# Optimization experiments

Measured on AMD Instinct MI355X. Metric: run time of the kernel, lower is better.

The kernel has to match this reference:

```python
import jax, jax.numpy as jnp
import numpy as np

N = 50000          # nodes
E = 800000         # edges (no self loops; self loops added in reference)
D = 128            # in_channels == out_channels (required by index_add into x)
HEADS = 1
NEG_SLOPE = 0.2
NUM_LABELS = 7


def setup_inputs() -> dict:
    key = jax.random.key(0)
    k0, k1, k2, k3, k4, k5 = jax.random.split(key, 6)
    x = jax.random.normal(k0, (N, D), dtype=jnp.float32)
    # edges guaranteed self-loop-free (remove_self_loops is then a no-op)
    src = jax.random.randint(k1, (E,), 0, N, dtype=jnp.int32)
    off = jax.random.randint(k2, (E,), 1, N, dtype=jnp.int32)
    dst = (src + off) % N
    edge_index = jnp.stack([src, dst])  # [2, E]
    node_label = jax.random.randint(k3, (N,), 0, 8, dtype=jnp.int32)  # 0 = inactive, 1..7 active
    glorot = float(np.sqrt(6.0 / (D + D)))
    weight_id = jax.random.uniform(k4, (NUM_LABELS, D, D), jnp.float32, -glorot, glorot)
    ga = float(np.sqrt(6.0 / (HEADS * 2 * D + 1)))
    att = jax.random.uniform(k5, (1, HEADS, 2 * D), jnp.float32, -ga, ga)
    return {"x": x, "edge_index": edge_index, "node_label": node_label,
            "weight_id": weight_id, "att": att}


def reference(x, edge_index, node_label, weight_id, att):
    n, d = x.shape
    # --- per-label identity transform: ox = x + W_{label-1} x for labels 1..7 ---
    y = jnp.einsum('nd,kdo->nko', x, weight_id)           # [N, 7, D]
    valid = (node_label >= 1) & (node_label <= NUM_LABELS)
    idx = jnp.clip(node_label - 1, 0, NUM_LABELS - 1)
    delta = jnp.take_along_axis(y, idx[:, None, None], axis=1)[:, 0]  # [N, D]
    ox = x + jnp.where(valid[:, None], delta, jnp.zeros_like(delta))
    # --- add self loops (input has none) ---
    loops = jnp.arange(n, dtype=edge_index.dtype)
    src = jnp.concatenate([edge_index[0], loops])
    dst = jnp.concatenate([edge_index[1], loops])
    # --- GAT message: gather, attention score, edge softmax over dst ---
    x_j = ox[src].reshape(-1, HEADS, d)                   # [Et, 1, D]
    x_i = ox[dst].reshape(-1, HEADS, d)
    alpha = (x_i * att[:, :, :d]).sum(-1) + (x_j * att[:, :, d:]).sum(-1)  # [Et, 1]
    alpha = jax.nn.leaky_relu(alpha, NEG_SLOPE)
    amax = jax.ops.segment_max(alpha, dst, num_segments=n)  # every node has a self loop
    alpha = jnp.exp(alpha - amax[dst])
    denom = jax.ops.segment_sum(alpha, dst, num_segments=n)
    alpha = alpha / (denom[dst] + 1e-16)
    # dropout p=0 (eval) -> no-op
    msg = (x_j * alpha[:, :, None]).reshape(-1, HEADS * d)  # concat=True, heads=1
    out = jax.ops.segment_sum(msg, dst, num_segments=n)     # [N, D]; bias=False
    return out
```

## Files before the change

### kernel.cpp

```cpp
#include <hip/hip_runtime.h>
#include <math.h>

#define N_NODES 50000
#define N_EDGES 800000
#define DIM 128
#define SCAN_BLOCKS ((N_NODES + 255) / 256)
#define DEG_CAP 48
#define BINS ((N_NODES + 255) / 256)
#define BIN_CAP 8192
#define EA_CHUNK 4096

#define PREP_ELEMS (N_NODES * DIM / 4 + 7 * DIM * DIM)
#define PREP_BLOCKS ((PREP_ELEMS + 255) / 256)
#define P1_GRID (BINS + PREP_BLOCKS + SCAN_BLOCKS)

#define TR_BLOCKS 784
#define P2_GRID (BINS + TR_BLOCKS)

typedef __attribute__((ext_vector_type(8))) short short8;
typedef __attribute__((ext_vector_type(4))) float floatx4;

__device__ __forceinline__ unsigned short f2bf(float f) {
    unsigned int u = __float_as_uint(f);
    unsigned int r = (u + 0x7fff + ((u >> 16) & 1)) >> 16;
    return (unsigned short)r;
}
__device__ __forceinline__ float bf2f_lo(unsigned int v) { return __uint_as_float(v << 16); }
__device__ __forceinline__ float bf2f_hi(unsigned int v) { return __uint_as_float(v & 0xffff0000u); }

__global__ __launch_bounds__(256) void phase1_kernel(
        const float* __restrict__ x, const int* __restrict__ src, const int* __restrict__ dst,
        const int* __restrict__ label, const float* __restrict__ W,
        unsigned short* __restrict__ oxh, unsigned short* __restrict__ Wt,
        int* __restrict__ bin_cur, unsigned int* __restrict__ binned,
        int* __restrict__ lab_cnt, int* __restrict__ node_list) {
    int t = threadIdx.x;
    int blk = blockIdx.x;

    if (blk < BINS) {
        __shared__ int hist[BINS], base_s[BINS], rank[BINS];
        for (int i = t; i < BINS; i += 256) { hist[i] = 0; rank[i] = 0; }
        __syncthreads();
        int e0 = blk * EA_CHUNK;
        int e1 = e0 + EA_CHUNK; if (e1 > N_EDGES) e1 = N_EDGES;
        for (int e = e0 + t; e < e1; e += 256) atomicAdd(&hist[dst[e] >> 8], 1);
        __syncthreads();
        for (int i = t; i < BINS; i += 256)
            base_s[i] = (hist[i] > 0) ? atomicAdd(&bin_cur[i], hist[i]) : 0;
        __syncthreads();
        for (int e = e0 + t; e < e1; e += 256) {
            int d = dst[e];
            int b = d >> 8;
            int r = atomicAdd(&rank[b], 1);
            int slot = base_s[b] + r;
            if (slot < BIN_CAP)
                binned[(size_t)b * BIN_CAP + slot] = (unsigned int)(src[e] | ((d & 255) << 16));
        }
    } else if (blk < BINS + PREP_BLOCKS) {
        int i = (blk - BINS) * 256 + t;
        const int nx = N_NODES * DIM / 4;
        if (i < nx) {
            float4 v = ((const float4*)x)[i];
            ushort4 o;
            o.x = f2bf(v.x); o.y = f2bf(v.y); o.z = f2bf(v.z); o.w = f2bf(v.w);
            ((ushort4*)oxh)[i] = o;
        } else {
            int j = i - nx;
            if (j < 7 * DIM * DIM) {
                int b = j >> 14;
                int d = (j >> 7) & 127;
                int c = j & 127;
                Wt[((size_t)b * DIM + c) * DIM + d] = f2bf(W[j]);
            }
        }
    } else {
        __shared__ int lcnt[8], lbase[8], lrank[8];
        int i = (blk - BINS - PREP_BLOCKS) * 256 + t;
        if (t < 8) { lcnt[t] = 0; lrank[t] = 0; }
        __syncthreads();
        int b = -1;
        if (i < N_NODES) {
            int lab = label[i];
            b = (lab >= 1 && lab <= 7) ? (lab - 1) : 7;
            atomicAdd(&lcnt[b], 1);
        }
        __syncthreads();
        if (t < 8) lbase[t] = (lcnt[t] > 0) ? atomicAdd(&lab_cnt[t], lcnt[t]) : 0;
        __syncthreads();
        if (i < N_NODES) {
            int r = atomicAdd(&lrank[b], 1);
            node_list[(size_t)b * N_NODES + lbase[b] + r] = i;
        }
    }
}

__global__ __launch_bounds__(256) void phase2_kernel(
        const float* __restrict__ x, const float* __restrict__ att,
        const int* __restrict__ lab_cnt, const int* __restrict__ node_list,
        const unsigned short* __restrict__ Wt,
        const int* __restrict__ bin_cur, const unsigned int* __restrict__ binned,
        unsigned short* __restrict__ oxh, float* __restrict__ ai, float* __restrict__ aj,
        int* __restrict__ cnt, unsigned short* __restrict__ bucket) {
    int t = threadIdx.x;
    int blk = blockIdx.x;

    if (blk < BINS) {
        __shared__ int hist[256], off[256], cur[256], sc[256];
        __shared__ unsigned short srt[BIN_CAP];
        int b = blk;
        int m = bin_cur[b]; if (m > BIN_CAP) m = BIN_CAP;
        const unsigned int* bp = binned + (size_t)b * BIN_CAP;

        hist[t] = 0; cur[t] = 0;
        __syncthreads();
        for (int i = t; i < m; i += 256) atomicAdd(&hist[(bp[i] >> 16) & 255], 1);
        __syncthreads();
        sc[t] = hist[t];
        __syncthreads();
        #pragma unroll
        for (int d = 1; d < 256; d <<= 1) {
            int add = (t >= d) ? sc[t - d] : 0;
            __syncthreads();
            sc[t] += add;
            __syncthreads();
        }
        off[t] = sc[t] - hist[t];
        __syncthreads();
        for (int i = t; i < m; i += 256) {
            unsigned int v = bp[i];
            int ln = (v >> 16) & 255;
            int r = atomicAdd(&cur[ln], 1);
            srt[off[ln] + r] = (unsigned short)(v & 0xFFFF);
        }
        __syncthreads();
        int n = b * 256 + t;
        if (n < N_NODES) {
            int deg = hist[t];
            if (deg > DEG_CAP) deg = DEG_CAP;
            cnt[n] = deg;
            int o = off[t];
            unsigned short* brow = bucket + (size_t)n * DEG_CAP;
            for (int k = 0; k < deg; k++) brow[k] = srt[o + k];
        }
    } else {
        int wv = t >> 6;
        int lane = t & 63;
        int tile = (blk - BINS) * 4 + wv;

        int b = 0, base = 0, tcnt = 0;
        for (; b < 8; b++) {
            int c = lab_cnt[b];
            int nt = (c + 15) >> 4;
            if (tile < nt) { base = b * N_NODES + tile * 16; tcnt = c - tile * 16; break; }
            tile -= nt;
        }
        if (b == 8) return;
        if (tcnt > 16) tcnt = 16;

        int m = lane & 15;
        int quad = lane >> 4;

        floatx4 acc[8];
        #pragma unroll
        for (int nt = 0; nt < 8; nt++) acc[nt] = (floatx4){0.f, 0.f, 0.f, 0.f};

        if (b < 7) {
            int mm = (m < tcnt) ? m : 0;
            int nodeA = node_list[base + mm];
            const unsigned short* xrow = oxh + (size_t)nodeA * DIM;
            short8 afrag[4];
            #pragma unroll
            for (int kk = 0; kk < 4; kk++)
                afrag[kk] = *(const short8*)(xrow + kk * 32 + quad * 8);

            const unsigned short* WtB = Wt + (size_t)b * DIM * DIM;
            #pragma unroll
            for (int kk = 0; kk < 4; kk++) {
                #pragma unroll
                for (int nt = 0; nt < 8; nt++) {
                    short8 bfrag = *(const short8*)(WtB + (size_t)(nt * 16 + m) * DIM + kk * 32 + quad * 8);
                    acc[nt] = __builtin_amdgcn_mfma_f32_16x16x32_bf16(afrag[kk], bfrag, acc[nt], 0, 0, 0);
                }
            }
        }

        int nodes[4];
        #pragma unroll
        for (int r = 0; r < 4; r++) {
            int rw = quad * 4 + r;
            nodes[r] = node_list[base + ((rw < tcnt) ? rw : 0)];
        }
        float pi[4] = {0.f, 0.f, 0.f, 0.f};
        float pj[4] = {0.f, 0.f, 0.f, 0.f};
        #pragma unroll
        for (int nt = 0; nt < 8; nt++) {
            int c = nt * 16 + m;
            float a1 = att[c];
            float a2 = att[DIM + c];
            #pragma unroll
            for (int r = 0; r < 4; r++) {
                int rw = quad * 4 + r;
                if (rw < tcnt) {
                    float xv = x[(size_t)nodes[r] * DIM + c];
                    float v = (b < 7) ? (acc[nt][r] + xv) : xv;
                    if (b < 7) oxh[(size_t)nodes[r] * DIM + c] = f2bf(v);
                    pi[r] += v * a1;
                    pj[r] += v * a2;
                }
            }
        }
        #pragma unroll
        for (int r = 0; r < 4; r++) {
            #pragma unroll
            for (int off = 1; off < 16; off <<= 1) {
                pi[r] += __shfl_xor(pi[r], off, 64);
                pj[r] += __shfl_xor(pj[r], off, 64);
            }
            int rw = quad * 4 + r;
            if (m == 0 && rw < tcnt) {
                ai[nodes[r]] = pi[r];
                aj[nodes[r]] = pj[r];
            }
        }
    }
}

__global__ __launch_bounds__(256) void gather6_kernel(
        const int* __restrict__ cnt, const unsigned short* __restrict__ bucket,
        const float* __restrict__ ai, const float* __restrict__ aj,
        const uint4* __restrict__ tab,
        float* __restrict__ out) {
    int wv = threadIdx.x >> 6;
    int lane = threadIdx.x & 63;
    int n = blockIdx.x * 4 + wv;
    if (n >= N_NODES) return;
    int deg = cnt[n];
    if (deg > DEG_CAP) deg = DEG_CAP;
    const unsigned short* row = bucket + (size_t)n * DEG_CAP;
    float ain = ai[n];

    float a = -INFINITY;
    int s = n;
    if (lane < deg) {
        s = row[lane];
        a = ain + aj[s];
        a = (a > 0.0f) ? a : 0.2f * a;
    } else if (lane == deg) {
        a = ain + aj[n];
        a = (a > 0.0f) ? a : 0.2f * a;
    }
    float mx = a;
    #pragma unroll
    for (int off = 32; off > 0; off >>= 1) mx = fmaxf(mx, __shfl_xor(mx, off, 64));
    float w = expf(a - mx);
    float ssum = w;
    #pragma unroll
    for (int off = 32; off > 0; off >>= 1) ssum += __shfl_xor(ssum, off, 64);
    float wn = w / (ssum + 1e-16f);
    float wsf = __shfl(wn, deg, 64);

    int g = lane >> 4;
    int cl = lane & 15;
    float ac0 = 0.f, ac1 = 0.f, ac2 = 0.f, ac3 = 0.f;
    float ac4 = 0.f, ac5 = 0.f, ac6 = 0.f, ac7 = 0.f;

    if (g == 0) {
        uint4 v = tab[(size_t)n * 16 + cl];
        ac0 += wsf * bf2f_lo(v.x); ac1 += wsf * bf2f_hi(v.x);
        ac2 += wsf * bf2f_lo(v.y); ac3 += wsf * bf2f_hi(v.y);
        ac4 += wsf * bf2f_lo(v.z); ac5 += wsf * bf2f_hi(v.z);
        ac6 += wsf * bf2f_lo(v.w); ac7 += wsf * bf2f_hi(v.w);
    }

    int niter = (deg + 3) >> 2;
    for (int k = 0; k < niter; k++) {
        int i = g + 4 * k;
        bool valid = (i < deg);
        int idx = valid ? i : 0;
        float wi = __shfl(wn, idx, 64);
        int   si = __shfl(s, idx, 64);
        if (!valid) wi = 0.0f;
        uint4 v = tab[(size_t)si * 16 + cl];
        ac0 += wi * bf2f_lo(v.x); ac1 += wi * bf2f_hi(v.x);
        ac2 += wi * bf2f_lo(v.y); ac3 += wi * bf2f_hi(v.y);
        ac4 += wi * bf2f_lo(v.z); ac5 += wi * bf2f_hi(v.z);
        ac6 += wi * bf2f_lo(v.w); ac7 += wi * bf2f_hi(v.w);
    }

    #pragma unroll
    for (int off = 16; off < 64; off <<= 1) {
        ac0 += __shfl_xor(ac0, off, 64); ac1 += __shfl_xor(ac1, off, 64);
        ac2 += __shfl_xor(ac2, off, 64); ac3 += __shfl_xor(ac3, off, 64);
        ac4 += __shfl_xor(ac4, off, 64); ac5 += __shfl_xor(ac5, off, 64);
        ac6 += __shfl_xor(ac6, off, 64); ac7 += __shfl_xor(ac7, off, 64);
    }
    if (g == 0) {
        float* op = out + (size_t)n * DIM + cl * 8;
        float4 o0; o0.x = ac0; o0.y = ac1; o0.z = ac2; o0.w = ac3;
        float4 o1; o1.x = ac4; o1.y = ac5; o1.z = ac6; o1.w = ac7;
        *(float4*)op = o0;
        *(float4*)(op + 4) = o1;
    }
}

extern "C" void kernel_launch(void* const* d_in, const int* in_sizes, int n_in,
                              void* d_out, int out_size, void* d_ws, size_t ws_size,
                              hipStream_t stream) {
    const float* x     = (const float*)d_in[0];
    const int*   ei    = (const int*)d_in[1];
    const int*   label = (const int*)d_in[2];
    const float* W     = (const float*)d_in[3];
    const float* att   = (const float*)d_in[4];
    float* out = (float*)d_out;

    const int* src = ei;
    const int* dst = ei + N_EDGES;

    char* w = (char*)d_ws;
    unsigned short* oxh    = (unsigned short*)w; w += sizeof(unsigned short) * (size_t)N_NODES * DIM;
    unsigned short* Wt     = (unsigned short*)w; w += sizeof(unsigned short) * 7 * DIM * DIM;
    unsigned short* bucket = (unsigned short*)w; w += sizeof(unsigned short) * (size_t)N_NODES * DEG_CAP;
    unsigned int*   binned = (unsigned int*)w;   w += sizeof(unsigned int) * (size_t)BINS * BIN_CAP;
    float* ai        = (float*)w;  w += sizeof(float) * N_NODES;
    float* aj        = (float*)w;  w += sizeof(float) * N_NODES;
    int*   cnt       = (int*)w;    w += sizeof(int) * N_NODES;
    int*   node_list = (int*)w;    w += sizeof(int) * (size_t)8 * N_NODES;
    int*   lab_cnt   = (int*)w;    w += sizeof(int) * 8;
    int*   bin_cur   = (int*)w;    w += sizeof(int) * BINS;

    hipMemsetAsync(lab_cnt, 0, sizeof(int) * (8 + BINS), stream);

    phase1_kernel<<<P1_GRID, 256, 0, stream>>>(x, src, dst, label, W,
                                               oxh, Wt, bin_cur, binned, lab_cnt, node_list);

    phase2_kernel<<<P2_GRID, 256, 0, stream>>>(x, att, lab_cnt, node_list, Wt,
                                               bin_cur, binned, oxh, ai, aj, cnt, bucket);

    gather6_kernel<<<(N_NODES + 3) / 4, 256, 0, stream>>>(cnt, bucket, ai, aj,
                                                          (const uint4*)oxh, out);
}
```

Baseline: 166.5 us.

## Replace two-pass binned CSR build with direct global-atomic bucket scatter

The edge bucketing drops the two-stage bin/local-sort path and has each edge do a global atomicAdd on a per-destination counter, writing its source straight into that node's fixed-capacity bucket. The separate x-to-bf16 conversion pass is also removed: the transform kernel converts x rows to bf16 on the fly for the MFMA A fragments and writes oxh for every node. This removes a kernel's worth of staging traffic and the intermediate binned buffer, at the cost of 800k contended global atomics and unordered bucket contents. The gather kernel now reads the raw counter, which can exceed DEG_CAP, and relies on its own clamp.

New measurement: 191.9 us. 15.3% more time.

```diff
diff --git a/kernel.cpp b/kernel.cpp
--- a/kernel.cpp
+++ b/kernel.cpp
@@ -4,18 +4,14 @@
 #define N_NODES 50000
 #define N_EDGES 800000
 #define DIM 128
-#define SCAN_BLOCKS ((N_NODES + 255) / 256)
 #define DEG_CAP 48
-#define BINS ((N_NODES + 255) / 256)
-#define BIN_CAP 8192
-#define EA_CHUNK 4096
-
-#define PREP_ELEMS (N_NODES * DIM / 4 + 7 * DIM * DIM)
-#define PREP_BLOCKS ((PREP_ELEMS + 255) / 256)
-#define P1_GRID (BINS + PREP_BLOCKS + SCAN_BLOCKS)
+
+#define SC_BLOCKS ((N_EDGES + 255) / 256)
+#define LB_BLOCKS ((N_NODES + 255) / 256)
+#define WT_BLOCKS ((7 * DIM * DIM + 255) / 256)
+#define K1_GRID (SC_BLOCKS + LB_BLOCKS + WT_BLOCKS)
 
 #define TR_BLOCKS 784
-#define P2_GRID (BINS + TR_BLOCKS)
 
 typedef __attribute__((ext_vector_type(8))) short short8;
 typedef __attribute__((ext_vector_type(4))) float floatx4;
@@ -28,54 +24,26 @@
 __device__ __forceinline__ float bf2f_lo(unsigned int v) { return __uint_as_float(v << 16); }
 __device__ __forceinline__ float bf2f_hi(unsigned int v) { return __uint_as_float(v & 0xffff0000u); }
 
-__global__ __launch_bounds__(256) void phase1_kernel(
-        const float* __restrict__ x, const int* __restrict__ src, const int* __restrict__ dst,
+__global__ __launch_bounds__(256) void build_kernel(
+        const int* __restrict__ src, const int* __restrict__ dst,
         const int* __restrict__ label, const float* __restrict__ W,
-        unsigned short* __restrict__ oxh, unsigned short* __restrict__ Wt,
-        int* __restrict__ bin_cur, unsigned int* __restrict__ binned,
+        unsigned short* __restrict__ Wt,
+        int* __restrict__ cur, unsigned short* __restrict__ bucket,
         int* __restrict__ lab_cnt, int* __restrict__ node_list) {
     int t = threadIdx.x;
     int blk = blockIdx.x;
 
-    if (blk < BINS) {
-        __shared__ int hist[BINS], base_s[BINS], rank[BINS];
-        for (int i = t; i < BINS; i += 256) { hist[i] = 0; rank[i] = 0; }
-        __syncthreads();
-        int e0 = blk * EA_CHUNK;
-        int e1 = e0 + EA_CHUNK; if (e1 > N_EDGES) e1 = N_EDGES;
-        for (int e = e0 + t; e < e1; e += 256) atomicAdd(&hist[dst[e] >> 8], 1);
-        __syncthreads();
-        for (int i = t; i < BINS; i += 256)
-            base_s[i] = (hist[i] > 0) ? atomicAdd(&bin_cur[i], hist[i]) : 0;
-        __syncthreads();
-        for (int e = e0 + t; e < e1; e += 256) {
+    if (blk < SC_BLOCKS) {
+        int e = blk * 256 + t;
+        if (e < N_EDGES) {
             int d = dst[e];
-            int b = d >> 8;
-            int r = atomicAdd(&rank[b], 1);
-            int slot = base_s[b] + r;
-            if (slot < BIN_CAP)
-                binned[(size_t)b * BIN_CAP + slot] = (unsigned int)(src[e] | ((d & 255) << 16));
-        }
-    } else if (blk < BINS + PREP_BLOCKS) {
-        int i = (blk - BINS) * 256 + t;
-        const int nx = N_NODES * DIM / 4;
-        if (i < nx) {
-            float4 v = ((const float4*)x)[i];
-            ushort4 o;
-            o.x = f2bf(v.x); o.y = f2bf(v.y); o.z = f2bf(v.z); o.w = f2bf(v.w);
-            ((ushort4*)oxh)[i] = o;
-        } else {
-            int j = i - nx;
-            if (j < 7 * DIM * DIM) {
-                int b = j >> 14;
-                int d = (j >> 7) & 127;
-                int c = j & 127;
-                Wt[((size_t)b * DIM + c) * DIM + d] = f2bf(W[j]);
-            }
-        }
-    } else {
+            int pos = atomicAdd(&cur[d], 1);
+            if (pos < DEG_CAP)
+                bucket[(size_t)d * DEG_CAP + pos] = (unsigned short)src[e];
+        }
+    } else if (blk < SC_BLOCKS + LB_BLOCKS) {
         __shared__ int lcnt[8], lbase[8], lrank[8];
-        int i = (blk - BINS - PREP_BLOCKS) * 256 + t;
+        int i = (blk - SC_BLOCKS) * 256 + t;
         if (t < 8) { lcnt[t] = 0; lrank[t] = 0; }
         __syncthreads();
         int b = -1;
@@ -91,136 +59,108 @@
             int r = atomicAdd(&lrank[b], 1);
             node_list[(size_t)b * N_NODES + lbase[b] + r] = i;
         }
-    }
-}
-
-__global__ __launch_bounds__(256) void phase2_kernel(
+    } else {
+        int j = (blk - SC_BLOCKS - LB_BLOCKS) * 256 + t;
+        if (j < 7 * DIM * DIM) {
+            int b = j >> 14;
+            int d = (j >> 7) & 127;
+            int c = j & 127;
+            Wt[((size_t)b * DIM + c) * DIM + d] = f2bf(W[j]);
+        }
+    }
+}
+
+__global__ __launch_bounds__(256) void transform_kernel(
         const float* __restrict__ x, const float* __restrict__ att,
         const int* __restrict__ lab_cnt, const int* __restrict__ node_list,
         const unsigned short* __restrict__ Wt,
-        const int* __restrict__ bin_cur, const unsigned int* __restrict__ binned,
-        unsigned short* __restrict__ oxh, float* __restrict__ ai, float* __restrict__ aj,
-        int* __restrict__ cnt, unsigned short* __restrict__ bucket) {
+        unsigned short* __restrict__ oxh, float* __restrict__ ai, float* __restrict__ aj) {
     int t = threadIdx.x;
-    int blk = blockIdx.x;
-
-    if (blk < BINS) {
-        __shared__ int hist[256], off[256], cur[256], sc[256];
-        __shared__ unsigned short srt[BIN_CAP];
-        int b = blk;
-        int m = bin_cur[b]; if (m > BIN_CAP) m = BIN_CAP;
-        const unsigned int* bp = binned + (size_t)b * BIN_CAP;
-
-        hist[t] = 0; cur[t] = 0;
-        __syncthreads();
-        for (int i = t; i < m; i += 256) atomicAdd(&hist[(bp[i] >> 16) & 255], 1);
-        __syncthreads();
-        sc[t] = hist[t];
-        __syncthreads();
-        #pragma unroll
-        for (int d = 1; d < 256; d <<= 1) {
-            int add = (t >= d) ? sc[t - d] : 0;
-            __syncthreads();
-            sc[t] += add;
-            __syncthreads();
-        }
-        off[t] = sc[t] - hist[t];
-        __syncthreads();
-        for (int i = t; i < m; i += 256) {
-            unsigned int v = bp[i];
-            int ln = (v >> 16) & 255;
-            int r = atomicAdd(&cur[ln], 1);
-            srt[off[ln] + r] = (unsigned short)(v & 0xFFFF);
-        }
-        __syncthreads();
-        int n = b * 256 + t;
-        if (n < N_NODES) {
-            int deg = hist[t];
-            if (deg > DEG_CAP) deg = DEG_CAP;
-            cnt[n] = deg;
-            int o = off[t];
-            unsigned short* brow = bucket + (size_t)n * DEG_CAP;
-            for (int k = 0; k < deg; k++) brow[k] = srt[o + k];
-        }
-    } else {
-        int wv = t >> 6;
-        int lane = t & 63;
-        int tile = (blk - BINS) * 4 + wv;
-
-        int b = 0, base = 0, tcnt = 0;
-        for (; b < 8; b++) {
-            int c = lab_cnt[b];
-            int nt = (c + 15) >> 4;
-            if (tile < nt) { base = b * N_NODES + tile * 16; tcnt = c - tile * 16; break; }
-            tile -= nt;
-        }
-        if (b == 8) return;
-        if (tcnt > 16) tcnt = 16;
-
-        int m = lane & 15;
-        int quad = lane >> 4;
-
-        floatx4 acc[8];
-        #pragma unroll
-        for (int nt = 0; nt < 8; nt++) acc[nt] = (floatx4){0.f, 0.f, 0.f, 0.f};
-
-        if (b < 7) {
-            int mm = (m < tcnt) ? m : 0;
-            int nodeA = node_list[base + mm];
-            const unsigned short* xrow = oxh + (size_t)nodeA * DIM;
-            short8 afrag[4];
+    int wv = t >> 6;
+    int lane = t & 63;
+    int tile = blockIdx.x * 4 + wv;
+
+    int b = 0, base = 0, tcnt = 0;
+    for (; b < 8; b++) {
+        int c = lab_cnt[b];
+        int nt = (c + 15) >> 4;
+        if (tile < nt) { base = b * N_NODES + tile * 16; tcnt = c - tile * 16; break; }
+        tile -= nt;
+    }
+    if (b == 8) return;
+    if (tcnt > 16) tcnt = 16;
+
+    int m = lane & 15;
+    int quad = lane >> 4;
+
+    floatx4 acc[8];
+    #pragma unroll
+    for (int nt = 0; nt < 8; nt++) acc[nt] = (floatx4){0.f, 0.f, 0.f, 0.f};
+
+    if (b < 7) {
+        int mm = (m < tcnt) ? m : 0;
+        int nodeA = node_list[base + mm];
+        const float* xrow = x + (size_t)nodeA * DIM;
+        short8 afrag[4];
+        #pragma unroll
+        for (int kk = 0; kk < 4; kk++) {
+            float4 f0 = *(const float4*)(xrow + kk * 32 + quad * 8);
+            float4 f1 = *(const float4*)(xrow + kk * 32 + quad * 8 + 4);
+            short8 a;
+            a[0] = (short)f2bf(f0.x); a[1] = (short)f2bf(f0.y);
+            a[2] = (short)f2bf(f0.z); a[3] = (short)f2bf(f0.w);
+            a[4] = (short)f2bf(f1.x); a[5] = (short)f2bf(f1.y);
+            a[6] = (short)f2bf(f1.z); a[7] = (short)f2bf(f1.w);
+            afrag[kk] = a;
+        }
+
+        const unsigned short* WtB = Wt + (size_t)b * DIM * DIM;
+        #pragma unroll
+        for (int kk = 0; kk < 4; kk++) {
             #pragma unroll
-            for (int kk = 0; kk < 4; kk++)
-                afrag[kk] = *(const short8*)(xrow + kk * 32 + quad * 8);
-
-            const unsigned short* WtB = Wt + (size_t)b * DIM * DIM;
-            #pragma unroll
-            for (int kk = 0; kk < 4; kk++) {
-                #pragma unroll
-                for (int nt = 0; nt < 8; nt++) {
-                    short8 bfrag = *(const short8*)(WtB + (size_t)(nt * 16 + m) * DIM + kk * 32 + quad * 8);
-                    acc[nt] = __builtin_amdgcn_mfma_f32_16x16x32_bf16(afrag[kk], bfrag, acc[nt], 0, 0, 0);
-                }
+            for (int nt = 0; nt < 8; nt++) {
+                short8 bfrag = *(const short8*)(WtB + (size_t)(nt * 16 + m) * DIM + kk * 32 + quad * 8);
+                acc[nt] = __builtin_amdgcn_mfma_f32_16x16x32_bf16(afrag[kk], bfrag, acc[nt], 0, 0, 0);
             }
         }
-
-        int nodes[4];
+    }
+
+    int nodes[4];
+    #pragma unroll
+    for (int r = 0; r < 4; r++) {
+        int rw = quad * 4 + r;
+        nodes[r] = node_list[base + ((rw < tcnt) ? rw : 0)];
+    }
+    float pi[4] = {0.f, 0.f, 0.f, 0.f};
+    float pj[4] = {0.f, 0.f, 0.f, 0.f};
+    #pragma unroll
+    for (int nt = 0; nt < 8; nt++) {
+        int c = nt * 16 + m;
+        float a1 = att[c];
+        float a2 = att[DIM + c];
         #pragma unroll
         for (int r = 0; r < 4; r++) {
             int rw = quad * 4 + r;
-            nodes[r] = node_list[base + ((rw < tcnt) ? rw : 0)];
-        }
-        float pi[4] = {0.f, 0.f, 0.f, 0.f};
-        float pj[4] = {0.f, 0.f, 0.f, 0.f};
-        #pragma unroll
-        for (int nt = 0; nt < 8; nt++) {
-            int c = nt * 16 + m;
-            float a1 = att[c];
-            float a2 = att[DIM + c];
-            #pragma unroll
-            for (int r = 0; r < 4; r++) {
-                int rw = quad * 4 + r;
-                if (rw < tcnt) {
-                    float xv = x[(size_t)nodes[r] * DIM + c];
-                    float v = (b < 7) ? (acc[nt][r] + xv) : xv;
-                    if (b < 7) oxh[(size_t)nodes[r] * DIM + c] = f2bf(v);
-                    pi[r] += v * a1;
-                    pj[r] += v * a2;
-                }
+            if (rw < tcnt) {
+                float xv = x[(size_t)nodes[r] * DIM + c];
+                float v = (b < 7) ? (acc[nt][r] + xv) : xv;
+                oxh[(size_t)nodes[r] * DIM + c] = f2bf(v);
+                pi[r] += v * a1;
+                pj[r] += v * a2;
             }
         }
-        #pragma unroll
-        for (int r = 0; r < 4; r++) {
-            #pragma unroll
-            for (int off = 1; off < 16; off <<= 1) {
-                pi[r] += __shfl_xor(pi[r], off, 64);
-                pj[r] += __shfl_xor(pj[r], off, 64);
-            }
-            int rw = quad * 4 + r;
-            if (m == 0 && rw < tcnt) {
-                ai[nodes[r]] = pi[r];
-                aj[nodes[r]] = pj[r];
-            }
+    }
+    #pragma unroll
+    for (int r = 0; r < 4; r++) {
+        #pragma unroll
+        for (int off = 1; off < 16; off <<= 1) {
+            pi[r] += __shfl_xor(pi[r], off, 64);
+            pj[r] += __shfl_xor(pj[r], off, 64);
+        }
+        int rw = quad * 4 + r;
+        if (m == 0 && rw < tcnt) {
+            ai[nodes[r]] = pi[r];
+            aj[nodes[r]] = pj[r];
         }
     }
 }
@@ -320,22 +260,20 @@
     unsigned short* oxh    = (unsigned short*)w; w += sizeof(unsigned short) * (size_t)N_NODES * DIM;
     unsigned short* Wt     = (unsigned short*)w; w += sizeof(unsigned short) * 7 * DIM * DIM;
     unsigned short* bucket = (unsigned short*)w; w += sizeof(unsigned short) * (size_t)N_NODES * DEG_CAP;
-    unsigned int*   binned = (unsigned int*)w;   w += sizeof(unsigned int) * (size_t)BINS * BIN_CAP;
     float* ai        = (float*)w;  w += sizeof(float) * N_NODES;
     float* aj        = (float*)w;  w += sizeof(float) * N_NODES;
-    int*   cnt       = (int*)w;    w += sizeof(int) * N_NODES;
     int*   node_list = (int*)w;    w += sizeof(int) * (size_t)8 * N_NODES;
     int*   lab_cnt   = (int*)w;    w += sizeof(int) * 8;
-    int*   bin_cur   = (int*)w;    w += sizeof(int) * BINS;
-
-    hipMemsetAsync(lab_cnt, 0, sizeof(int) * (8 + BINS), stream);
-
-    phase1_kernel<<<P1_GRID, 256, 0, stream>>>(x, src, dst, label, W,
-                                               oxh, Wt, bin_cur, binned, lab_cnt, node_list);
-
-    phase2_kernel<<<P2_GRID, 256, 0, stream>>>(x, att, lab_cnt, node_list, Wt,
-                                               bin_cur, binned, oxh, ai, aj, cnt, bucket);
-
-    gather6_kernel<<<(N_NODES + 3) / 4, 256, 0, stream>>>(cnt, bucket, ai, aj,
+    int*   cur       = (int*)w;    w += sizeof(int) * N_NODES;
+
+    hipMemsetAsync(lab_cnt, 0, sizeof(int) * (8 + N_NODES), stream);
+
+    build_kernel<<<K1_GRID, 256, 0, stream>>>(src, dst, label, W,
+                                              Wt, cur, bucket, lab_cnt, node_list);
+
+    transform_kernel<<<TR_BLOCKS, 256, 0, stream>>>(x, att, lab_cnt, node_list, Wt,
+                                                    oxh, ai, aj);
+
+    gather6_kernel<<<(N_NODES + 3) / 4, 256, 0, stream>>>(cur, bucket, ai, aj,
                                                           (const uint4*)oxh, out);
 }
```

## Drop bf16 x prepass, bucket edges directly in LDS rows, rebalance edge chunks

Applied to the files above, without the earlier changes.

Removes the separate pass that converted all of x to bf16. The MFMA tiles now read fp32 x and convert it in registers, and they write oxh for every node, including unlabeled ones. The per-bin counting sort with prefix scan is replaced by direct atomic slot insertion into a fixed 256xDEG_CAP LDS row buffer, which is then copied out with coalesced uint4 stores. The edge chunk size changes so the number of binning blocks is decoupled from BINS. Neighbor order within a bucket becomes nondeterministic, and fp32 x is read twice in the transform tiles.

Result: no change. 166.6 us (+0.0%).

```diff
diff --git a/kernel.cpp b/kernel.cpp
--- a/kernel.cpp
+++ b/kernel.cpp
@@ -4,18 +4,18 @@
 #define N_NODES 50000
 #define N_EDGES 800000
 #define DIM 128
-#define SCAN_BLOCKS ((N_NODES + 255) / 256)
 #define DEG_CAP 48
 #define BINS ((N_NODES + 255) / 256)
 #define BIN_CAP 8192
-#define EA_CHUNK 4096
-
-#define PREP_ELEMS (N_NODES * DIM / 4 + 7 * DIM * DIM)
-#define PREP_BLOCKS ((PREP_ELEMS + 255) / 256)
-#define P1_GRID (BINS + PREP_BLOCKS + SCAN_BLOCKS)
+#define EA_CHUNK 3125
+#define BA_BLOCKS ((N_EDGES + EA_CHUNK - 1) / EA_CHUNK)
+
+#define LB_BLOCKS ((N_NODES + 255) / 256)
+#define WT_BLOCKS ((7 * DIM * DIM + 255) / 256)
+#define K1_GRID (BA_BLOCKS + LB_BLOCKS + WT_BLOCKS)
 
 #define TR_BLOCKS 784
-#define P2_GRID (BINS + TR_BLOCKS)
+#define K2_GRID (BINS + TR_BLOCKS)
 
 typedef __attribute__((ext_vector_type(8))) short short8;
 typedef __attribute__((ext_vector_type(4))) float floatx4;
@@ -28,16 +28,16 @@
 __device__ __forceinline__ float bf2f_lo(unsigned int v) { return __uint_as_float(v << 16); }
 __device__ __forceinline__ float bf2f_hi(unsigned int v) { return __uint_as_float(v & 0xffff0000u); }
 
-__global__ __launch_bounds__(256) void phase1_kernel(
-        const float* __restrict__ x, const int* __restrict__ src, const int* __restrict__ dst,
+__global__ __launch_bounds__(256) void build_kernel(
+        const int* __restrict__ src, const int* __restrict__ dst,
         const int* __restrict__ label, const float* __restrict__ W,
-        unsigned short* __restrict__ oxh, unsigned short* __restrict__ Wt,
+        unsigned short* __restrict__ Wt,
         int* __restrict__ bin_cur, unsigned int* __restrict__ binned,
         int* __restrict__ lab_cnt, int* __restrict__ node_list) {
     int t = threadIdx.x;
     int blk = blockIdx.x;
 
-    if (blk < BINS) {
+    if (blk < BA_BLOCKS) {
         __shared__ int hist[BINS], base_s[BINS], rank[BINS];
         for (int i = t; i < BINS; i += 256) { hist[i] = 0; rank[i] = 0; }
         __syncthreads();
@@ -56,26 +56,9 @@
             if (slot < BIN_CAP)
                 binned[(size_t)b * BIN_CAP + slot] = (unsigned int)(src[e] | ((d & 255) << 16));
         }
-    } else if (blk < BINS + PREP_BLOCKS) {
-        int i = (blk - BINS) * 256 + t;
-        const int nx = N_NODES * DIM / 4;
-        if (i < nx) {
-            float4 v = ((const float4*)x)[i];
-            ushort4 o;
-            o.x = f2bf(v.x); o.y = f2bf(v.y); o.z = f2bf(v.z); o.w = f2bf(v.w);
-            ((ushort4*)oxh)[i] = o;
-        } else {
-            int j = i - nx;
-            if (j < 7 * DIM * DIM) {
-                int b = j >> 14;
-                int d = (j >> 7) & 127;
-                int c = j & 127;
-                Wt[((size_t)b * DIM + c) * DIM + d] = f2bf(W[j]);
-            }
-        }
-    } else {
+    } else if (blk < BA_BLOCKS + LB_BLOCKS) {
         __shared__ int lcnt[8], lbase[8], lrank[8];
-        int i = (blk - BINS - PREP_BLOCKS) * 256 + t;
+        int i = (blk - BA_BLOCKS) * 256 + t;
         if (t < 8) { lcnt[t] = 0; lrank[t] = 0; }
         __syncthreads();
         int b = -1;
@@ -90,6 +73,14 @@
         if (i < N_NODES) {
             int r = atomicAdd(&lrank[b], 1);
             node_list[(size_t)b * N_NODES + lbase[b] + r] = i;
+        }
+    } else {
+        int j = (blk - BA_BLOCKS - LB_BLOCKS) * 256 + t;
+        if (j < 7 * DIM * DIM) {
+            int b = j >> 14;
+            int d = (j >> 7) & 127;
+            int c = j & 127;
+            Wt[((size_t)b * DIM + c) * DIM + d] = f2bf(W[j]);
         }
     }
 }
@@ -105,43 +96,32 @@
     int blk = blockIdx.x;
 
     if (blk < BINS) {
-        __shared__ int hist[256], off[256], cur[256], sc[256];
-        __shared__ unsigned short srt[BIN_CAP];
+        __shared__ unsigned short rows[256][DEG_CAP];
+        __shared__ int lcnt[256];
         int b = blk;
         int m = bin_cur[b]; if (m > BIN_CAP) m = BIN_CAP;
         const unsigned int* bp = binned + (size_t)b * BIN_CAP;
 
-        hist[t] = 0; cur[t] = 0;
-        __syncthreads();
-        for (int i = t; i < m; i += 256) atomicAdd(&hist[(bp[i] >> 16) & 255], 1);
-        __syncthreads();
-        sc[t] = hist[t];
-        __syncthreads();
-        #pragma unroll
-        for (int d = 1; d < 256; d <<= 1) {
-            int add = (t >= d) ? sc[t - d] : 0;
-            __syncthreads();
-            sc[t] += add;
-            __syncthreads();
-        }
-        off[t] = sc[t] - hist[t];
+        lcnt[t] = 0;
         __syncthreads();
         for (int i = t; i < m; i += 256) {
             unsigned int v = bp[i];
             int ln = (v >> 16) & 255;
-            int r = atomicAdd(&cur[ln], 1);
-            srt[off[ln] + r] = (unsigned short)(v & 0xFFFF);
+            int p = atomicAdd(&lcnt[ln], 1);
+            if (p < DEG_CAP) rows[ln][p] = (unsigned short)(v & 0xFFFF);
         }
         __syncthreads();
         int n = b * 256 + t;
         if (n < N_NODES) {
-            int deg = hist[t];
+            int deg = lcnt[t];
             if (deg > DEG_CAP) deg = DEG_CAP;
             cnt[n] = deg;
-            int o = off[t];
-            unsigned short* brow = bucket + (size_t)n * DEG_CAP;
-            for (int k = 0; k < deg; k++) brow[k] = srt[o + k];
-        }
+        }
+        uint4* gdst = (uint4*)(bucket + (size_t)b * 256 * DEG_CAP);
+        const uint4* lsrc = (const uint4*)rows;
+        #pragma unroll
+        for (int k = 0; k < (256 * DEG_CAP * 2 / 16) / 256; k++)
+            gdst[t + k * 256] = lsrc[t + k * 256];
     } else {
         int wv = t >> 6;
         int lane = t & 63;
@@ -167,11 +147,19 @@
         if (b < 7) {
             int mm = (m < tcnt) ? m : 0;
             int nodeA = node_list[base + mm];
-            const unsigned short* xrow = oxh + (size_t)nodeA * DIM;
+            const float* xrow = x + (size_t)nodeA * DIM;
             short8 afrag[4];
             #pragma unroll
-            for (int kk = 0; kk < 4; kk++)
-                afrag[kk] = *(const short8*)(xrow + kk * 32 + quad * 8);
+            for (int kk = 0; kk < 4; kk++) {
+                float4 f0 = *(const float4*)(xrow + kk * 32 + quad * 8);
+                float4 f1 = *(const float4*)(xrow + kk * 32 + quad * 8 + 4);
+                short8 a;
+                a[0] = (short)f2bf(f0.x); a[1] = (short)f2bf(f0.y);
+                a[2] = (short)f2bf(f0.z); a[3] = (short)f2bf(f0.w);
+                a[4] = (short)f2bf(f1.x); a[5] = (short)f2bf(f1.y);
+                a[6] = (short)f2bf(f1.z); a[7] = (short)f2bf(f1.w);
+                afrag[kk] = a;
+            }
 
             const unsigned short* WtB = Wt + (size_t)b * DIM * DIM;
             #pragma unroll
@@ -203,7 +191,7 @@
                 if (rw < tcnt) {
                     float xv = x[(size_t)nodes[r] * DIM + c];
                     float v = (b < 7) ? (acc[nt][r] + xv) : xv;
-                    if (b < 7) oxh[(size_t)nodes[r] * DIM + c] = f2bf(v);
+                    oxh[(size_t)nodes[r] * DIM + c] = f2bf(v);
                     pi[r] += v * a1;
                     pj[r] += v * a2;
                 }
@@ -319,7 +307,7 @@
     char* w = (char*)d_ws;
     unsigned short* oxh    = (unsigned short*)w; w += sizeof(unsigned short) * (size_t)N_NODES * DIM;
     unsigned short* Wt     = (unsigned short*)w; w += sizeof(unsigned short) * 7 * DIM * DIM;
-    unsigned short* bucket = (unsigned short*)w; w += sizeof(unsigned short) * (size_t)N_NODES * DEG_CAP;
+    unsigned short* bucket = (unsigned short*)w; w += sizeof(unsigned short) * (size_t)BINS * 256 * DEG_CAP;
     unsigned int*   binned = (unsigned int*)w;   w += sizeof(unsigned int) * (size_t)BINS * BIN_CAP;
     float* ai        = (float*)w;  w += sizeof(float) * N_NODES;
     float* aj        = (float*)w;  w += sizeof(float) * N_NODES;
@@ -330,10 +318,10 @@
 
     hipMemsetAsync(lab_cnt, 0, sizeof(int) * (8 + BINS), stream);
 
-    phase1_kernel<<<P1_GRID, 256, 0, stream>>>(x, src, dst, label, W,
-                                               oxh, Wt, bin_cur, binned, lab_cnt, node_list);
-
-    phase2_kernel<<<P2_GRID, 256, 0, stream>>>(x, att, lab_cnt, node_list, Wt,
+    build_kernel<<<K1_GRID, 256, 0, stream>>>(src, dst, label, W,
+                                              Wt, bin_cur, binned, lab_cnt, node_list);
+
+    phase2_kernel<<<K2_GRID, 256, 0, stream>>>(x, att, lab_cnt, node_list, Wt,
                                                bin_cur, binned, oxh, ai, aj, cnt, bucket);
 
     gather6_kernel<<<(N_NODES + 3) / 4, 256, 0, stream>>>(cnt, bucket, ai, aj,
```
